# Kernel tuning notes

Measured on AMD Instinct MI355X. Metric: run time of the kernel, lower is better.

## Reference

```python
import jax, jax.numpy as jnp
import numpy as np

N = 100000
E = 1600000
D = 64
ETA = 0.5
NEG_SLOPE = 0.01  # torch F.leaky_relu default


def setup_inputs() -> dict:
    key = jax.random.key(0)
    ks = jax.random.split(key, 6)
    h = jax.random.normal(ks[0], (N, D), dtype=jnp.float32)
    tax = jax.random.normal(ks[1], (N, D), dtype=jnp.float32)
    src = jax.random.randint(ks[2], (E,), 0, N, dtype=jnp.int32)
    dst = jax.random.randint(ks[3], (E,), 0, N, dtype=jnp.int32)
    # xavier_normal for Linear weights
    wh_w = jax.random.normal(ks[4], (1, 2 * D), dtype=jnp.float32) * np.sqrt(2.0 / (2 * D + 1))
    W_w = jax.random.normal(ks[5], (D, D), dtype=jnp.float32) * np.sqrt(2.0 / (D + D))
    W_b = jnp.zeros((D,), dtype=jnp.float32)
    return {"h": h, "tax": tax, "src": src, "dst": dst,
            "wh_w": wh_w, "W_w": W_w, "W_b": W_b}


def _edge_softmax(logits, dst):
    # logits: [E, 1]; softmax over edges grouped by destination node
    m = jax.ops.segment_max(logits, dst, num_segments=N)            # [N, 1]
    m = jnp.where(jnp.isfinite(m), m, 0.0)                          # nodes w/o in-edges
    e = jnp.exp(logits - m[dst])                                    # [E, 1]
    s = jax.ops.segment_sum(e, dst, num_segments=N)                 # [N, 1]
    return e / s[dst]


def reference(h, tax, src, dst, wh_w, W_w, W_b):
    hs, hd = h[src], h[dst]                                         # [E, D] gathers
    wf = jax.nn.leaky_relu(jnp.concatenate([hs, hd], axis=1) @ wh_w.T,
                           negative_slope=NEG_SLOPE)                # [E, 1]
    alpha_f = _edge_softmax(wf, dst)
    wt = jnp.sum(tax[src] * tax[dst], axis=1, keepdims=True)        # [E, 1]
    alpha_t = _edge_softmax(wt, dst)
    alpha = ETA * alpha_f + (1.0 - ETA) * alpha_t                   # [E, 1]
    z = jax.ops.segment_sum(hs * alpha, dst, num_segments=N)        # [N, D]
    return z @ W_w.T + W_b
```

## Files before the change

### kernel.cpp

```cpp
#include <hip/hip_runtime.h>

#define NEG_SLOPE 0.01f
#define ETA 0.5f
#define NEG_BIG -3.402823466e38f
#define LOG2E 1.4426950408889634f
#define PCHUNK 16384
#define CAP 1536
#define NBMAX 1568
#define GSTRIDE 16

typedef _Float16 half2v __attribute__((ext_vector_type(2)));
typedef _Float16 half8v __attribute__((ext_vector_type(8)));
typedef float f32x4v __attribute__((ext_vector_type(4)));

#if defined(__has_builtin)
#if __has_builtin(__builtin_amdgcn_fdot2)
#define HAVE_FDOT2 1
#endif
#if __has_builtin(__builtin_amdgcn_exp2f)
#define HAVE_EXP2 1
#endif
#if __has_builtin(__builtin_amdgcn_update_dpp)
#define HAVE_DPP 1
#endif
#if __has_builtin(__builtin_amdgcn_mfma_f32_16x16x32_f16)
#define HAVE_MFMA16 1
#endif
#endif

__device__ __forceinline__ float fdot2(half2v a, half2v b, float c) {
#ifdef HAVE_FDOT2
  return __builtin_amdgcn_fdot2(a, b, c, false);
#else
  return (float)a[0] * (float)b[0] + (float)a[1] * (float)b[1] + c;
#endif
}

__device__ __forceinline__ unsigned pack2(float x, float y) {
  half2v h = {( _Float16)x, (_Float16)y};
  return __builtin_bit_cast(unsigned, h);
}

__device__ __forceinline__ float fexp2(float x) {
#ifdef HAVE_EXP2
  return __builtin_amdgcn_exp2f(x);
#else
  return __expf(x * 0.6931471805599453f);
#endif
}

__device__ __forceinline__ void rowsum16x2(float& x, float& y) {
#ifdef HAVE_DPP
#define DPPADD(v, ctl)                                                        \
  v += __builtin_bit_cast(float, __builtin_amdgcn_update_dpp(                 \
         0, __builtin_bit_cast(int, v), ctl, 0xf, 0xf, true))
  DPPADD(x, 0x121); DPPADD(y, 0x121);
  DPPADD(x, 0x122); DPPADD(y, 0x122);
  DPPADD(x, 0x124); DPPADD(y, 0x124);
  DPPADD(x, 0x128); DPPADD(y, 0x128);
#undef DPPADD
#else
#pragma unroll
  for (int o = 1; o < 16; o <<= 1) {
    x += __shfl_xor(x, o);
    y += __shfl_xor(y, o);
  }
#endif
}

__device__ __forceinline__ void prep_body(const float* __restrict__ h,
                                          const float* __restrict__ tax,
                                          const float* __restrict__ whw,
                                          float* __restrict__ af, float* __restrict__ bf,
                                          uint4* __restrict__ rec, int n, int blk) {
  int gid = blk * 256 + (int)threadIdx.x;
  int node = gid >> 4, lane = gid & 15;
  if (node >= n) return;
  float4 x  = ((const float4*)(h + (size_t)node * 64))[lane];
  float4 tx = ((const float4*)(tax + (size_t)node * 64))[lane];
  float4 wa = ((const float4*)whw)[lane];
  float4 wb = ((const float4*)(whw + 64))[lane];
  uint4 r;
  r.x = pack2(tx.x, tx.y);
  r.y = pack2(tx.z, tx.w);
  r.z = pack2(x.x, x.y);
  r.w = pack2(x.z, x.w);
  rec[((size_t)node << 4) + lane] = r;
  float pa = x.x * wa.x + x.y * wa.y + x.z * wa.z + x.w * wa.w;
  float pb = x.x * wb.x + x.y * wb.y + x.z * wb.z + x.w * wb.w;
#pragma unroll
  for (int o = 8; o; o >>= 1) {
    pa += __shfl_xor(pa, o);
    pb += __shfl_xor(pb, o);
  }
  if (lane == 0) { af[node] = pa * LOG2E; bf[node] = pb * LOG2E; }
}

__device__ __forceinline__ void part_body(const int* __restrict__ src,
                                          const int* __restrict__ dst,
                                          int* __restrict__ gcur, int* __restrict__ pck,
                                          int ne, int nb, int blk) {
  __shared__ int s_hist[NBMAX];
  int t = threadIdx.x;
  int base = blk * PCHUNK;
  int cnt = ne - base; if (cnt > PCHUNK) cnt = PCHUNK;
  for (int j = t; j < nb; j += 256) s_hist[j] = 0;
  __syncthreads();
  int i = t * 4;
  for (; i + 3 < cnt; i += 1024) {
    int4 dd = *(const int4*)(dst + base + i);
    atomicAdd(&s_hist[dd.x >> 6], 1);
    atomicAdd(&s_hist[dd.y >> 6], 1);
    atomicAdd(&s_hist[dd.z >> 6], 1);
    atomicAdd(&s_hist[dd.w >> 6], 1);
  }
  for (; i < cnt; ++i) atomicAdd(&s_hist[dst[base + i] >> 6], 1);
  __syncthreads();
  for (int j = t; j < nb; j += 256) {
    int v = s_hist[j];
    if (v > 0) s_hist[j] = atomicAdd(&gcur[j * GSTRIDE], v);
  }
  __syncthreads();
  i = t * 4;
  for (; i + 3 < cnt; i += 1024) {
    int4 dd = *(const int4*)(dst + base + i);
    int4 ss = *(const int4*)(src + base + i);
    int r, g;
    r = dd.x >> 6; g = atomicAdd(&s_hist[r], 1);
    if (g < CAP) pck[(size_t)r * CAP + g] = (ss.x << 6) | (dd.x & 63);
    r = dd.y >> 6; g = atomicAdd(&s_hist[r], 1);
    if (g < CAP) pck[(size_t)r * CAP + g] = (ss.y << 6) | (dd.y & 63);
    r = dd.z >> 6; g = atomicAdd(&s_hist[r], 1);
    if (g < CAP) pck[(size_t)r * CAP + g] = (ss.z << 6) | (dd.z & 63);
    r = dd.w >> 6; g = atomicAdd(&s_hist[r], 1);
    if (g < CAP) pck[(size_t)r * CAP + g] = (ss.w << 6) | (dd.w & 63);
  }
  for (; i < cnt; ++i) {
    int d = dst[base + i];
    int r = d >> 6;
    int g = atomicAdd(&s_hist[r], 1);
    if (g < CAP) pck[(size_t)r * CAP + g] = (src[base + i] << 6) | (d & 63);
  }
}

__global__ void k_prep_part(const float* __restrict__ h, const float* __restrict__ tax,
                            const float* __restrict__ whw,
                            float* __restrict__ af, float* __restrict__ bf,
                            uint4* __restrict__ rec,
                            const int* __restrict__ src, const int* __restrict__ dst,
                            int* __restrict__ gcur, int* __restrict__ pck,
                            int n, int ne, int nb, int npart) {
  int b = (int)blockIdx.x;
  if (b < npart) part_body(src, dst, gcur, pck, ne, nb, b);
  else           prep_body(h, tax, whw, af, bf, rec, n, b - npart);
}

__launch_bounds__(256)
__global__ void k_fused(const uint4* __restrict__ rec,
                        const float* __restrict__ af, const float* __restrict__ bf,
                        const int* __restrict__ gcur, const int* __restrict__ pck,
                        unsigned short* __restrict__ z, int n) {
  __shared__ int s_hist[64];
  __shared__ int s_off[65];
  __shared__ int s_cur[64];
  __shared__ int s_srcs[CAP];
  int b = (int)blockIdx.x;
  int t = (int)threadIdx.x;
  int cnt = gcur[b * GSTRIDE]; if (cnt > CAP) cnt = CAP;
  const int* pb = pck + (size_t)b * CAP;
  if (t < 64) s_hist[t] = 0;
  __syncthreads();
  for (int i = t; i < cnt; i += 256) atomicAdd(&s_hist[pb[i] & 63], 1);
  __syncthreads();
  if (t < 64) {
    int x = s_hist[t];
#pragma unroll
    for (int o = 1; o < 64; o <<= 1) {
      int y = __shfl_up(x, o);
      if (t >= o) x += y;
    }
    s_off[t + 1] = x;
    if (t == 0) s_off[0] = 0;
  }
  __syncthreads();
  if (t < 64) s_cur[t] = s_off[t];
  __syncthreads();
  for (int i = t; i < cnt; i += 256) {
    int p = pb[i];
    int r = atomicAdd(&s_cur[p & 63], 1);
    s_srcs[r] = p >> 6;
  }
  __syncthreads();
  int g = t >> 4, q = t & 15;
#pragma unroll
  for (int rnd = 0; rnd < 4; ++rnd) {
    int ld = g + (rnd << 4);
    int d = (b << 6) + ld;
    if (d >= n) continue;
    uint2 rd = *(const uint2*)((const char*)rec + ((((size_t)d << 4) + q) << 4));
    half2v d01 = __builtin_bit_cast(half2v, rd.x);
    half2v d23 = __builtin_bit_cast(half2v, rd.y);
    float bfd = bf[d];
    int beg = s_off[ld], end = s_off[ld + 1];
    float sf = 0.f, st = 0.f, mt = NEG_BIG;
    float zf0 = 0.f, zf1 = 0.f, zf2 = 0.f, zf3 = 0.f;
    float zt0 = 0.f, zt1 = 0.f, zt2 = 0.f, zt3 = 0.f;
    int s0 = (beg     < end) ? s_srcs[beg]     : 0;
    int s1 = (beg + 1 < end) ? s_srcs[beg + 1] : 0;
    uint4 r0 = rec[((size_t)s0 << 4) + q];
    float a0 = af[s0];
    uint4 r1 = rec[((size_t)s1 << 4) + q];
    float a1 = af[s1];
    int s2 = (beg + 2 < end) ? s_srcs[beg + 2] : 0;
    int s3 = (beg + 3 < end) ? s_srcs[beg + 3] : 0;
    for (int i = beg; i < end; i += 2) {
      uint4 rn0 = rec[((size_t)s2 << 4) + q];
      float an0 = af[s2];
      uint4 rn1 = rec[((size_t)s3 << 4) + q];
      float an1 = af[s3];
      int s4 = (i + 4 < end) ? s_srcs[i + 4] : 0;
      int s5 = (i + 5 < end) ? s_srcs[i + 5] : 0;
      half2v t01a = __builtin_bit_cast(half2v, r0.x);
      half2v t23a = __builtin_bit_cast(half2v, r0.y);
      half2v h01a = __builtin_bit_cast(half2v, r0.z);
      half2v h23a = __builtin_bit_cast(half2v, r0.w);
      half2v t01b = __builtin_bit_cast(half2v, r1.x);
      half2v t23b = __builtin_bit_cast(half2v, r1.y);
      half2v h01b = __builtin_bit_cast(half2v, r1.z);
      half2v h23b = __builtin_bit_cast(half2v, r1.w);
      float p0 = fdot2(t23a, d23, fdot2(t01a, d01, 0.f)) * LOG2E;
      float p1 = fdot2(t23b, d23, fdot2(t01b, d01, 0.f)) * LOG2E;
      rowsum16x2(p0, p1);
      float wf0 = a0 + bfd;
      wf0 = (wf0 > 0.f) ? wf0 : NEG_SLOPE * wf0;
      float wf1 = a1 + bfd;
      wf1 = (wf1 > 0.f) ? wf1 : NEG_SLOPE * wf1;
      if (i + 1 >= end) { p1 = -1e30f; wf1 = -1e30f; }
      float ef0 = fexp2(wf0), ef1 = fexp2(wf1);
      sf += ef0 + ef1;
      zf0 = fmaf((float)h01b[0], ef1, fmaf((float)h01a[0], ef0, zf0));
      zf1 = fmaf((float)h01b[1], ef1, fmaf((float)h01a[1], ef0, zf1));
      zf2 = fmaf((float)h23b[0], ef1, fmaf((float)h23a[0], ef0, zf2));
      zf3 = fmaf((float)h23b[1], ef1, fmaf((float)h23a[1], ef0, zf3));
      float pm0 = p0 - mt;
      if (pm0 > 60.f) {
        float sc = fexp2(-pm0);
        st *= sc;
        zt0 *= sc; zt1 *= sc; zt2 *= sc; zt3 *= sc;
        mt = p0; pm0 = 0.f;
      }
      float et0 = fexp2(pm0);
      st += et0;
      zt0 = fmaf((float)h01a[0], et0, zt0);
      zt1 = fmaf((float)h01a[1], et0, zt1);
      zt2 = fmaf((float)h23a[0], et0, zt2);
      zt3 = fmaf((float)h23a[1], et0, zt3);
      float pm1 = p1 - mt;
      if (pm1 > 60.f) {
        float sc = fexp2(-pm1);
        st *= sc;
        zt0 *= sc; zt1 *= sc; zt2 *= sc; zt3 *= sc;
        mt = p1; pm1 = 0.f;
      }
      float et1 = fexp2(pm1);
      st += et1;
      zt0 = fmaf((float)h01b[0], et1, zt0);
      zt1 = fmaf((float)h01b[1], et1, zt1);
      zt2 = fmaf((float)h23b[0], et1, zt2);
      zt3 = fmaf((float)h23b[1], et1, zt3);
      r0 = rn0; a0 = an0; r1 = rn1; a1 = an1;
      s2 = s4;  s3 = s5;
    }
    float4 zv = make_float4(0.f, 0.f, 0.f, 0.f);
    if (end > beg) {
      float rf = ETA / sf, rt = (1.f - ETA) / st;
      zv.x = rf * zf0 + rt * zt0;
      zv.y = rf * zf1 + rt * zt1;
      zv.z = rf * zf2 + rt * zt2;
      zv.w = rf * zf3 + rt * zt3;
    }
    uint2 zo;
    zo.x = pack2(zv.x, zv.y);
    zo.y = pack2(zv.z, zv.w);
    ((uint2*)(z + (size_t)d * 64))[q] = zo;
  }
}

#ifdef HAVE_MFMA16
__launch_bounds__(256)
__global__ void k_out_gemm(const unsigned short* __restrict__ z,
                           const float* __restrict__ W,
                           const float* __restrict__ b, float* __restrict__ out, int n) {
  int l = threadIdx.x & 63;
  int wv = threadIdx.x >> 6;
  int c16 = l & 15;
  int seg = l >> 4;
  half8v bh[4][2], bl[4][2];
#pragma unroll
  for (int jt = 0; jt < 4; ++jt) {
    const float* wr = W + (size_t)(jt * 16 + c16) * 64 + seg * 8;
#pragma unroll
    for (int ks = 0; ks < 2; ++ks) {
      const float* wk = wr + ks * 32;
#pragma unroll
      for (int e = 0; e < 8; ++e) {
        float wvv = wk[e];
        _Float16 hi = (_Float16)wvv;
        bh[jt][ks][e] = hi;
        bl[jt][ks][e] = (_Float16)(wvv - (float)hi);
      }
    }
  }
  float bias0 = b[c16], bias1 = b[16 + c16], bias2 = b[32 + c16], bias3 = b[48 + c16];
  const half8v* z8 = (const half8v*)z;
  int tiles = (n + 15) >> 4;
  int nw = (int)gridDim.x * 4;
  for (int t = (int)blockIdx.x * 4 + wv; t < tiles; t += nw) {
    int base = t << 4;
    int arow = base + c16;
    size_t zi = (size_t)(arow < n ? arow : n - 1) * 8 + seg;
    half8v a0 = z8[zi];
    half8v a1 = z8[zi + 4];
    f32x4v acc0 = {bias0, bias0, bias0, bias0};
    f32x4v acc1 = {bias1, bias1, bias1, bias1};
    f32x4v acc2 = {bias2, bias2, bias2, bias2};
    f32x4v acc3 = {bias3, bias3, bias3, bias3};
    acc0 = __builtin_amdgcn_mfma_f32_16x16x32_f16(a0, bh[0][0], acc0, 0, 0, 0);
    acc1 = __builtin_amdgcn_mfma_f32_16x16x32_f16(a0, bh[1][0], acc1, 0, 0, 0);
    acc2 = __builtin_amdgcn_mfma_f32_16x16x32_f16(a0, bh[2][0], acc2, 0, 0, 0);
    acc3 = __builtin_amdgcn_mfma_f32_16x16x32_f16(a0, bh[3][0], acc3, 0, 0, 0);
    acc0 = __builtin_amdgcn_mfma_f32_16x16x32_f16(a1, bh[0][1], acc0, 0, 0, 0);
    acc1 = __builtin_amdgcn_mfma_f32_16x16x32_f16(a1, bh[1][1], acc1, 0, 0, 0);
    acc2 = __builtin_amdgcn_mfma_f32_16x16x32_f16(a1, bh[2][1], acc2, 0, 0, 0);
    acc3 = __builtin_amdgcn_mfma_f32_16x16x32_f16(a1, bh[3][1], acc3, 0, 0, 0);
    acc0 = __builtin_amdgcn_mfma_f32_16x16x32_f16(a0, bl[0][0], acc0, 0, 0, 0);
    acc1 = __builtin_amdgcn_mfma_f32_16x16x32_f16(a0, bl[1][0], acc1, 0, 0, 0);
    acc2 = __builtin_amdgcn_mfma_f32_16x16x32_f16(a0, bl[2][0], acc2, 0, 0, 0);
    acc3 = __builtin_amdgcn_mfma_f32_16x16x32_f16(a0, bl[3][0], acc3, 0, 0, 0);
    acc0 = __builtin_amdgcn_mfma_f32_16x16x32_f16(a1, bl[0][1], acc0, 0, 0, 0);
    acc1 = __builtin_amdgcn_mfma_f32_16x16x32_f16(a1, bl[1][1], acc1, 0, 0, 0);
    acc2 = __builtin_amdgcn_mfma_f32_16x16x32_f16(a1, bl[2][1], acc2, 0, 0, 0);
    acc3 = __builtin_amdgcn_mfma_f32_16x16x32_f16(a1, bl[3][1], acc3, 0, 0, 0);
#pragma unroll
    for (int r = 0; r < 4; ++r) {
      int nrow = base + seg * 4 + r;
      if (nrow < n) {
        float* o = out + (size_t)nrow * 64 + c16;
        o[0]  = acc0[r];
        o[16] = acc1[r];
        o[32] = acc2[r];
        o[48] = acc3[r];
      }
    }
  }
}
#else
__launch_bounds__(256)
__global__ void k_out_gemm(const unsigned short* __restrict__ z,
                           const float* __restrict__ W,
                           const float* __restrict__ b, float* __restrict__ out, int n) {
  int t = threadIdx.x;
  int j = t & 63, nl = t >> 6;
  float wreg[64];
#pragma unroll
  for (int i = 0; i < 16; ++i)
    ((float4*)wreg)[i] = ((const float4*)(W + (size_t)j * 64))[i];
  float bias = b[j];
  int stride = gridDim.x * 4;
  for (int node = blockIdx.x * 4 + nl; node < n; node += stride) {
    float zv = (float)__builtin_bit_cast(_Float16, z[(size_t)node * 64 + j]);
    float acc = bias;
#pragma unroll
    for (int k = 0; k < 64; ++k)
      acc += __shfl(zv, k) * wreg[k];
    out[(size_t)node * 64 + j] = acc;
  }
}
#endif

extern "C" void kernel_launch(void* const* d_in, const int* in_sizes, int n_in,
                              void* d_out, int out_size, void* d_ws, size_t ws_size,
                              hipStream_t stream) {
  const float* h   = (const float*)d_in[0];
  const float* tax = (const float*)d_in[1];
  const int*   src = (const int*)d_in[2];
  const int*   dst = (const int*)d_in[3];
  const float* whw = (const float*)d_in[4];
  const float* Ww  = (const float*)d_in[5];
  const float* Wb  = (const float*)d_in[6];
  float* out = (float*)d_out;
  int n  = in_sizes[0] / 64;
  int ne = in_sizes[2];
  int nb = (n + 63) >> 6;

  float* af   = (float*)d_ws;
  float* bf   = af + n;
  int*   gcur = (int*)(bf + n);
  size_t w = (size_t)(2 * n) + (size_t)NBMAX * GSTRIDE;
  w = (w + 3) & ~(size_t)3;
  unsigned short* z = (unsigned short*)((int*)d_ws + w);
  uint4* rec = (uint4*)(z + (size_t)n * 64);
  int* pck = (int*)d_out;

  int nprep = (n * 16 + 255) / 256;
  int npart = (ne + PCHUNK - 1) / PCHUNK;
  int bg    = (((n + 15) >> 4) + 3) / 4;

  hipMemsetAsync(gcur, 0, (size_t)nb * GSTRIDE * sizeof(int), stream);
  k_prep_part<<<npart + nprep, 256, 0, stream>>>(h, tax, whw, af, bf, rec,
                                                 src, dst, gcur, pck, n, ne, nb, npart);
  k_fused<<<nb, 256, 0, stream>>>(rec, af, bf, gcur, pck, z, n);
  k_out_gemm<<<bg, 256, 0, stream>>>(z, Ww, Wb, out, n);
}
```

Before: 229.9 us.

## Fuse output linear projection into aggregation kernel via shared-memory MFMA

```diff
diff --git a/kernel.cpp b/kernel.cpp
--- a/kernel.cpp
+++ b/kernel.cpp
@@ -8,6 +8,7 @@
 #define CAP 1536
 #define NBMAX 1568
 #define GSTRIDE 16
+#define ZPAD 36
 
 typedef _Float16 half2v __attribute__((ext_vector_type(2)));
 typedef _Float16 half8v __attribute__((ext_vector_type(8)));
@@ -159,11 +160,13 @@
 __global__ void k_fused(const uint4* __restrict__ rec,
                         const float* __restrict__ af, const float* __restrict__ bf,
                         const int* __restrict__ gcur, const int* __restrict__ pck,
-                        unsigned short* __restrict__ z, int n) {
+                        const float* __restrict__ W, const float* __restrict__ bias,
+                        float* __restrict__ out, int n) {
   __shared__ int s_hist[64];
   __shared__ int s_off[65];
   __shared__ int s_cur[64];
   __shared__ int s_srcs[CAP];
+  __shared__ unsigned s_zu[64 * ZPAD];
   int b = (int)blockIdx.x;
   int t = (int)threadIdx.x;
   int cnt = gcur[b * GSTRIDE]; if (cnt > CAP) cnt = CAP;
@@ -196,187 +199,155 @@
   for (int rnd = 0; rnd < 4; ++rnd) {
     int ld = g + (rnd << 4);
     int d = (b << 6) + ld;
-    if (d >= n) continue;
-    uint2 rd = *(const uint2*)((const char*)rec + ((((size_t)d << 4) + q) << 4));
-    half2v d01 = __builtin_bit_cast(half2v, rd.x);
-    half2v d23 = __builtin_bit_cast(half2v, rd.y);
-    float bfd = bf[d];
-    int beg = s_off[ld], end = s_off[ld + 1];
-    float sf = 0.f, st = 0.f, mt = NEG_BIG;
-    float zf0 = 0.f, zf1 = 0.f, zf2 = 0.f, zf3 = 0.f;
-    float zt0 = 0.f, zt1 = 0.f, zt2 = 0.f, zt3 = 0.f;
-    int s0 = (beg     < end) ? s_srcs[beg]     : 0;
-    int s1 = (beg + 1 < end) ? s_srcs[beg + 1] : 0;
-    uint4 r0 = rec[((size_t)s0 << 4) + q];
-    float a0 = af[s0];
-    uint4 r1 = rec[((size_t)s1 << 4) + q];
-    float a1 = af[s1];
-    int s2 = (beg + 2 < end) ? s_srcs[beg + 2] : 0;
-    int s3 = (beg + 3 < end) ? s_srcs[beg + 3] : 0;
-    for (int i = beg; i < end; i += 2) {
-      uint4 rn0 = rec[((size_t)s2 << 4) + q];
-      float an0 = af[s2];
-      uint4 rn1 = rec[((size_t)s3 << 4) + q];
-      float an1 = af[s3];
-      int s4 = (i + 4 < end) ? s_srcs[i + 4] : 0;
-      int s5 = (i + 5 < end) ? s_srcs[i + 5] : 0;
-      half2v t01a = __builtin_bit_cast(half2v, r0.x);
-      half2v t23a = __builtin_bit_cast(half2v, r0.y);
-      half2v h01a = __builtin_bit_cast(half2v, r0.z);
-      half2v h23a = __builtin_bit_cast(half2v, r0.w);
-      half2v t01b = __builtin_bit_cast(half2v, r1.x);
-      half2v t23b = __builtin_bit_cast(half2v, r1.y);
-      half2v h01b = __builtin_bit_cast(half2v, r1.z);
-      half2v h23b = __builtin_bit_cast(half2v, r1.w);
-      float p0 = fdot2(t23a, d23, fdot2(t01a, d01, 0.f)) * LOG2E;
-      float p1 = fdot2(t23b, d23, fdot2(t01b, d01, 0.f)) * LOG2E;
-      rowsum16x2(p0, p1);
-      float wf0 = a0 + bfd;
-      wf0 = (wf0 > 0.f) ? wf0 : NEG_SLOPE * wf0;
-      float wf1 = a1 + bfd;
-      wf1 = (wf1 > 0.f) ? wf1 : NEG_SLOPE * wf1;
-      if (i + 1 >= end) { p1 = -1e30f; wf1 = -1e30f; }
-      float ef0 = fexp2(wf0), ef1 = fexp2(wf1);
-      sf += ef0 + ef1;
-      zf0 = fmaf((float)h01b[0], ef1, fmaf((float)h01a[0], ef0, zf0));
-      zf1 = fmaf((float)h01b[1], ef1, fmaf((float)h01a[1], ef0, zf1));
-      zf2 = fmaf((float)h23b[0], ef1, fmaf((float)h23a[0], ef0, zf2));
-      zf3 = fmaf((float)h23b[1], ef1, fmaf((float)h23a[1], ef0, zf3));
-      float pm0 = p0 - mt;
-      if (pm0 > 60.f) {
-        float sc = fexp2(-pm0);
-        st *= sc;
-        zt0 *= sc; zt1 *= sc; zt2 *= sc; zt3 *= sc;
-        mt = p0; pm0 = 0.f;
-      }
-      float et0 = fexp2(pm0);
-      st += et0;
-      zt0 = fmaf((float)h01a[0], et0, zt0);
-      zt1 = fmaf((float)h01a[1], et0, zt1);
-      zt2 = fmaf((float)h23a[0], et0, zt2);
-      zt3 = fmaf((float)h23a[1], et0, zt3);
-      float pm1 = p1 - mt;
-      if (pm1 > 60.f) {
-        float sc = fexp2(-pm1);
-        st *= sc;
-        zt0 *= sc; zt1 *= sc; zt2 *= sc; zt3 *= sc;
-        mt = p1; pm1 = 0.f;
-      }
-      float et1 = fexp2(pm1);
-      st += et1;
-      zt0 = fmaf((float)h01b[0], et1, zt0);
-      zt1 = fmaf((float)h01b[1], et1, zt1);
-      zt2 = fmaf((float)h23b[0], et1, zt2);
-      zt3 = fmaf((float)h23b[1], et1, zt3);
-      r0 = rn0; a0 = an0; r1 = rn1; a1 = an1;
-      s2 = s4;  s3 = s5;
+    float4 zv = make_float4(0.f, 0.f, 0.f, 0.f);
+    if (d < n) {
+      uint2 rd = *(const uint2*)((const char*)rec + ((((size_t)d << 4) + q) << 4));
+      half2v d01 = __builtin_bit_cast(half2v, rd.x);
+      half2v d23 = __builtin_bit_cast(half2v, rd.y);
+      float bfd = bf[d];
+      int beg = s_off[ld], end = s_off[ld + 1];
+      float sf = 0.f, st = 0.f, mt = NEG_BIG;
+      float zf0 = 0.f, zf1 = 0.f, zf2 = 0.f, zf3 = 0.f;
+      float zt0 = 0.f, zt1 = 0.f, zt2 = 0.f, zt3 = 0.f;
+      int s0 = (beg     < end) ? s_srcs[beg]     : 0;
+      int s1 = (beg + 1 < end) ? s_srcs[beg + 1] : 0;
+      uint4 r0 = rec[((size_t)s0 << 4) + q];
+      float a0 = af[s0];
+      uint4 r1 = rec[((size_t)s1 << 4) + q];
+      float a1 = af[s1];
+      int s2 = (beg + 2 < end) ? s_srcs[beg + 2] : 0;
+      int s3 = (beg + 3 < end) ? s_srcs[beg + 3] : 0;
+      for (int i = beg; i < end; i += 2) {
+        uint4 rn0 = rec[((size_t)s2 << 4) + q];
+        float an0 = af[s2];
+        uint4 rn1 = rec[((size_t)s3 << 4) + q];
+        float an1 = af[s3];
+        int s4 = (i + 4 < end) ? s_srcs[i + 4] : 0;
+        int s5 = (i + 5 < end) ? s_srcs[i + 5] : 0;
+        half2v t01a = __builtin_bit_cast(half2v, r0.x);
+        half2v t23a = __builtin_bit_cast(half2v, r0.y);
+        half2v h01a = __builtin_bit_cast(half2v, r0.z);
+        half2v h23a = __builtin_bit_cast(half2v, r0.w);
+        half2v t01b = __builtin_bit_cast(half2v, r1.x);
+        half2v t23b = __builtin_bit_cast(half2v, r1.y);
+        half2v h01b = __builtin_bit_cast(half2v, r1.z);
+        half2v h23b = __builtin_bit_cast(half2v, r1.w);
+        float p0 = fdot2(t23a, d23, fdot2(t01a, d01, 0.f)) * LOG2E;
+        float p1 = fdot2(t23b, d23, fdot2(t01b, d01, 0.f)) * LOG2E;
+        rowsum16x2(p0, p1);
+        float wf0 = a0 + bfd;
+        wf0 = (wf0 > 0.f) ? wf0 : NEG_SLOPE * wf0;
+        float wf1 = a1 + bfd;
+        wf1 = (wf1 > 0.f) ? wf1 : NEG_SLOPE * wf1;
+        if (i + 1 >= end) { p1 = -1e30f; wf1 = -1e30f; }
+        float ef0 = fexp2(wf0), ef1 = fexp2(wf1);
+        sf += ef0 + ef1;
+        zf0 = fmaf((float)h01b[0], ef1, fmaf((float)h01a[0], ef0, zf0));
+        zf1 = fmaf((float)h01b[1], ef1, fmaf((float)h01a[1], ef0, zf1));
+        zf2 = fmaf((float)h23b[0], ef1, fmaf((float)h23a[0], ef0, zf2));
+        zf3 = fmaf((float)h23b[1], ef1, fmaf((float)h23a[1], ef0, zf3));
+        float pm0 = p0 - mt;
+        if (pm0 > 60.f) {
+          float sc = fexp2(-pm0);
+          st *= sc;
+          zt0 *= sc; zt1 *= sc; zt2 *= sc; zt3 *= sc;
+          mt = p0; pm0 = 0.f;
+        }
+        float et0 = fexp2(pm0);
+        st += et0;
+        zt0 = fmaf((float)h01a[0], et0, zt0);
+        zt1 = fmaf((float)h01a[1], et0, zt1);
+        zt2 = fmaf((float)h23a[0], et0, zt2);
+        zt3 = fmaf((float)h23a[1], et0, zt3);
+        float pm1 = p1 - mt;
+        if (pm1 > 60.f) {
+          float sc = fexp2(-pm1);
+          st *= sc;
+          zt0 *= sc; zt1 *= sc; zt2 *= sc; zt3 *= sc;
+          mt = p1; pm1 = 0.f;
+        }
+        float et1 = fexp2(pm1);
+        st += et1;
+        zt0 = fmaf((float)h01b[0], et1, zt0);
+        zt1 = fmaf((float)h01b[1], et1, zt1);
+        zt2 = fmaf((float)h23b[0], et1, zt2);
+        zt3 = fmaf((float)h23b[1], et1, zt3);
+        r0 = rn0; a0 = an0; r1 = rn1; a1 = an1;
+        s2 = s4;  s3 = s5;
+      }
+      if (end > beg) {
+        float rf = ETA / sf, rt = (1.f - ETA) / st;
+        zv.x = rf * zf0 + rt * zt0;
+        zv.y = rf * zf1 + rt * zt1;
+        zv.z = rf * zf2 + rt * zt2;
+        zv.w = rf * zf3 + rt * zt3;
+      }
     }
-    float4 zv = make_float4(0.f, 0.f, 0.f, 0.f);
-    if (end > beg) {
-      float rf = ETA / sf, rt = (1.f - ETA) / st;
-      zv.x = rf * zf0 + rt * zt0;
-      zv.y = rf * zf1 + rt * zt1;
-      zv.z = rf * zf2 + rt * zt2;
-      zv.w = rf * zf3 + rt * zt3;
+    s_zu[ld * ZPAD + 2 * q]     = pack2(zv.x, zv.y);
+    s_zu[ld * ZPAD + 2 * q + 1] = pack2(zv.z, zv.w);
+  }
+  __syncthreads();
+#ifdef HAVE_MFMA16
+  {
+    int l = t & 63, wv = t >> 6;
+    int c16 = l & 15, seg = l >> 4;
+    int rbase = wv << 4;
+    const unsigned* za = s_zu + (size_t)(rbase + c16) * ZPAD;
+    half8v a0 = __builtin_bit_cast(half8v, *(const uint4*)(za + seg * 4));
+    half8v a1 = __builtin_bit_cast(half8v, *(const uint4*)(za + 16 + seg * 4));
+#pragma unroll
+    for (int jt = 0; jt < 4; ++jt) {
+      int j = (jt << 4) + c16;
+      const float* wr = W + (size_t)j * 64 + seg * 8;
+      half8v bh0, bl0, bh1, bl1;
+#pragma unroll
+      for (int e = 0; e < 8; ++e) {
+        float w0 = wr[e];
+        _Float16 hi0 = (_Float16)w0;
+        bh0[e] = hi0; bl0[e] = (_Float16)(w0 - (float)hi0);
+        float w1 = wr[32 + e];
+        _Float16 hi1 = (_Float16)w1;
+        bh1[e] = hi1; bl1[e] = (_Float16)(w1 - (float)hi1);
+      }
+      float bj = bias[j];
+      f32x4v acc = {bj, bj, bj, bj};
+      acc = __builtin_amdgcn_mfma_f32_16x16x32_f16(a0, bh0, acc, 0, 0, 0);
+      acc = __builtin_amdgcn_mfma_f32_16x16x32_f16(a1, bh1, acc, 0, 0, 0);
+      acc = __builtin_amdgcn_mfma_f32_16x16x32_f16(a0, bl0, acc, 0, 0, 0);
+      acc = __builtin_amdgcn_mfma_f32_16x16x32_f16(a1, bl1, acc, 0, 0, 0);
+#pragma unroll
+      for (int r = 0; r < 4; ++r) {
+        int nrow = (b << 6) + rbase + (seg << 2) + r;
+        if (nrow < n) out[(size_t)nrow * 64 + j] = acc[r];
+      }
     }
-    uint2 zo;
-    zo.x = pack2(zv.x, zv.y);
-    zo.y = pack2(zv.z, zv.w);
-    ((uint2*)(z + (size_t)d * 64))[q] = zo;
-  }
-}
-
-#ifdef HAVE_MFMA16
-__launch_bounds__(256)
-__global__ void k_out_gemm(const unsigned short* __restrict__ z,
-                           const float* __restrict__ W,
-                           const float* __restrict__ b, float* __restrict__ out, int n) {
-  int l = threadIdx.x & 63;
-  int wv = threadIdx.x >> 6;
-  int c16 = l & 15;
-  int seg = l >> 4;
-  half8v bh[4][2], bl[4][2];
-#pragma unroll
-  for (int jt = 0; jt < 4; ++jt) {
-    const float* wr = W + (size_t)(jt * 16 + c16) * 64 + seg * 8;
-#pragma unroll
-    for (int ks = 0; ks < 2; ++ks) {
-      const float* wk = wr + ks * 32;
-#pragma unroll
-      for (int e = 0; e < 8; ++e) {
-        float wvv = wk[e];
-        _Float16 hi = (_Float16)wvv;
-        bh[jt][ks][e] = hi;
-        bl[jt][ks][e] = (_Float16)(wvv - (float)hi);
+  }
+#else
+  {
+    int l = t & 63, wv = t >> 6;
+    int c16 = l & 15, seg = l >> 4;
+    int rbase = wv << 4;
+#pragma unroll
+    for (int jt = 0; jt < 4; ++jt) {
+      int j = (jt << 4) + c16;
+#pragma unroll
+      for (int r = 0; r < 4; ++r) {
+        int lrow = rbase + (seg << 2) + r;
+        int nrow = (b << 6) + lrow;
+        if (nrow >= n) continue;
+        float acc = bias[j];
+        const unsigned* zr = s_zu + (size_t)lrow * ZPAD;
+        for (int k = 0; k < 32; ++k) {
+          half2v hv = __builtin_bit_cast(half2v, zr[k]);
+          acc += (float)hv[0] * W[(size_t)j * 64 + 2 * k]
+               + (float)hv[1] * W[(size_t)j * 64 + 2 * k + 1];
+        }
+        out[(size_t)nrow * 64 + j] = acc;
       }
     }
   }
-  float bias0 = b[c16], bias1 = b[16 + c16], bias2 = b[32 + c16], bias3 = b[48 + c16];
-  const half8v* z8 = (const half8v*)z;
-  int tiles = (n + 15) >> 4;
-  int nw = (int)gridDim.x * 4;
-  for (int t = (int)blockIdx.x * 4 + wv; t < tiles; t += nw) {
-    int base = t << 4;
-    int arow = base + c16;
-    size_t zi = (size_t)(arow < n ? arow : n - 1) * 8 + seg;
-    half8v a0 = z8[zi];
-    half8v a1 = z8[zi + 4];
-    f32x4v acc0 = {bias0, bias0, bias0, bias0};
-    f32x4v acc1 = {bias1, bias1, bias1, bias1};
-    f32x4v acc2 = {bias2, bias2, bias2, bias2};
-    f32x4v acc3 = {bias3, bias3, bias3, bias3};
-    acc0 = __builtin_amdgcn_mfma_f32_16x16x32_f16(a0, bh[0][0], acc0, 0, 0, 0);
-    acc1 = __builtin_amdgcn_mfma_f32_16x16x32_f16(a0, bh[1][0], acc1, 0, 0, 0);
-    acc2 = __builtin_amdgcn_mfma_f32_16x16x32_f16(a0, bh[2][0], acc2, 0, 0, 0);
-    acc3 = __builtin_amdgcn_mfma_f32_16x16x32_f16(a0, bh[3][0], acc3, 0, 0, 0);
-    acc0 = __builtin_amdgcn_mfma_f32_16x16x32_f16(a1, bh[0][1], acc0, 0, 0, 0);
-    acc1 = __builtin_amdgcn_mfma_f32_16x16x32_f16(a1, bh[1][1], acc1, 0, 0, 0);
-    acc2 = __builtin_amdgcn_mfma_f32_16x16x32_f16(a1, bh[2][1], acc2, 0, 0, 0);
-    acc3 = __builtin_amdgcn_mfma_f32_16x16x32_f16(a1, bh[3][1], acc3, 0, 0, 0);
-    acc0 = __builtin_amdgcn_mfma_f32_16x16x32_f16(a0, bl[0][0], acc0, 0, 0, 0);
-    acc1 = __builtin_amdgcn_mfma_f32_16x16x32_f16(a0, bl[1][0], acc1, 0, 0, 0);
-    acc2 = __builtin_amdgcn_mfma_f32_16x16x32_f16(a0, bl[2][0], acc2, 0, 0, 0);
-    acc3 = __builtin_amdgcn_mfma_f32_16x16x32_f16(a0, bl[3][0], acc3, 0, 0, 0);
-    acc0 = __builtin_amdgcn_mfma_f32_16x16x32_f16(a1, bl[0][1], acc0, 0, 0, 0);
-    acc1 = __builtin_amdgcn_mfma_f32_16x16x32_f16(a1, bl[1][1], acc1, 0, 0, 0);
-    acc2 = __builtin_amdgcn_mfma_f32_16x16x32_f16(a1, bl[2][1], acc2, 0, 0, 0);
-    acc3 = __builtin_amdgcn_mfma_f32_16x16x32_f16(a1, bl[3][1], acc3, 0, 0, 0);
-#pragma unroll
-    for (int r = 0; r < 4; ++r) {
-      int nrow = base + seg * 4 + r;
-      if (nrow < n) {
-        float* o = out + (size_t)nrow * 64 + c16;
-        o[0]  = acc0[r];
-        o[16] = acc1[r];
-        o[32] = acc2[r];
-        o[48] = acc3[r];
-      }
-    }
-  }
-}
-#else
-__launch_bounds__(256)
-__global__ void k_out_gemm(const unsigned short* __restrict__ z,
-                           const float* __restrict__ W,
-                           const float* __restrict__ b, float* __restrict__ out, int n) {
-  int t = threadIdx.x;
-  int j = t & 63, nl = t >> 6;
-  float wreg[64];
-#pragma unroll
-  for (int i = 0; i < 16; ++i)
-    ((float4*)wreg)[i] = ((const float4*)(W + (size_t)j * 64))[i];
-  float bias = b[j];
-  int stride = gridDim.x * 4;
-  for (int node = blockIdx.x * 4 + nl; node < n; node += stride) {
-    float zv = (float)__builtin_bit_cast(_Float16, z[(size_t)node * 64 + j]);
-    float acc = bias;
-#pragma unroll
-    for (int k = 0; k < 64; ++k)
-      acc += __shfl(zv, k) * wreg[k];
-    out[(size_t)node * 64 + j] = acc;
-  }
-}
-#endif
+#endif
+}
 
 extern "C" void kernel_launch(void* const* d_in, const int* in_sizes, int n_in,
                               void* d_out, int out_size, void* d_ws, size_t ws_size,
@@ -396,19 +367,16 @@
   float* af   = (float*)d_ws;
   float* bf   = af + n;
   int*   gcur = (int*)(bf + n);
-  size_t w = (size_t)(2 * n) + (size_t)NBMAX * GSTRIDE;
+  int*   pck  = gcur + (size_t)NBMAX * GSTRIDE;
+  size_t w = (size_t)(2 * n) + (size_t)NBMAX * GSTRIDE + (size_t)nb * CAP;
   w = (w + 3) & ~(size_t)3;
-  unsigned short* z = (unsigned short*)((int*)d_ws + w);
-  uint4* rec = (uint4*)(z + (size_t)n * 64);
-  int* pck = (int*)d_out;
+  uint4* rec = (uint4*)((int*)d_ws + w);
 
   int nprep = (n * 16 + 255) / 256;
   int npart = (ne + PCHUNK - 1) / PCHUNK;
-  int bg    = (((n + 15) >> 4) + 3) / 4;
 
   hipMemsetAsync(gcur, 0, (size_t)nb * GSTRIDE * sizeof(int), stream);
   k_prep_part<<<npart + nprep, 256, 0, stream>>>(h, tax, whw, af, bf, rec,
                                                  src, dst, gcur, pck, n, ne, nb, npart);
-  k_fused<<<nb, 256, 0, stream>>>(rec, af, bf, gcur, pck, z, n);
-  k_out_gemm<<<bg, 256, 0, stream>>>(z, Ww, Wb, out, n);
-}
+  k_fused<<<nb, 256, 0, stream>>>(rec, af, bf, gcur, pck, Ww, Wb, out, n);
+}
```

After: 219.3 us. -4.6%, faster.
